# Kernel tuning notes

Measured on AMD Instinct MI355X. Metric: run time of the kernel, lower is better.

## Reference

```python
import jax, jax.numpy as jnp
import numpy as np

B, T, D = 256, 336, 128
H = 1024
N_LABEL, LABEL_CLASS = 24, 1
FORGET_BIAS = 1.0  # TF BasicLSTMCell default


def setup_inputs() -> dict:
    key = jax.random.key(0)
    ks = jax.random.split(key, 8)
    s1 = 1.0 / np.sqrt(D + H)
    s2 = 1.0 / np.sqrt(2 * H)
    sd = 1.0 / np.sqrt(H)
    return {
        "features": jax.random.normal(ks[0], (B, T, D), jnp.float32),
        "labels": jax.random.normal(ks[1], (B, N_LABEL, LABEL_CLASS), jnp.float32),
        "W1": jax.random.normal(ks[2], (D + H, 4 * H), jnp.float32) * s1,
        "b1": jnp.zeros((4 * H,), jnp.float32),
        "W2": jax.random.normal(ks[3], (2 * H, 4 * H), jnp.float32) * s2,
        "b2": jnp.zeros((4 * H,), jnp.float32),
        "Wd": jax.random.normal(ks[4], (H, N_LABEL * LABEL_CLASS), jnp.float32) * sd,
        "bd": jnp.zeros((N_LABEL * LABEL_CLASS,), jnp.float32),
    }


def _lstm_cell(c, h, x, W, b):
    # TF BasicLSTMCell: gates = [x, h] @ W + b, split into i, j, f, o
    z = jnp.concatenate([x, h], axis=-1) @ W + b
    i, j, f, o = jnp.split(z, 4, axis=-1)
    new_c = c * jax.nn.sigmoid(f + FORGET_BIAS) + jax.nn.sigmoid(i) * jnp.tanh(j)
    new_h = jnp.tanh(new_c) * jax.nn.sigmoid(o)
    return new_c, new_h


def reference(features, labels, W1, b1, W2, b2, Wd, bd):
    batch = features.shape[0]
    zeros = jnp.zeros((batch, H), features.dtype)
    init = (zeros, zeros, zeros, zeros)  # c1, h1, c2, h2

    def step(carry, x_t):
        c1, h1, c2, h2 = carry
        c1, h1 = _lstm_cell(c1, h1, x_t, W1, b1)
        c2, h2 = _lstm_cell(c2, h2, h1, W2, b2)
        return (c1, h1, c2, h2), None

    xs = jnp.swapaxes(features, 0, 1)  # [T, B, D]
    (c1, h1, c2, h2), _ = jax.lax.scan(step, init, xs)
    # dense head on last-timestep output of top layer
    pred = (h2 @ Wd + bd).reshape(batch, N_LABEL, LABEL_CLASS)
    loss = jnp.mean(jnp.square(pred - labels))
    return loss
```

## Files before the change

### kernel.cpp

```cpp
#include <hip/hip_runtime.h>

#define TT 336
#define BB 256
#define DD 128
#define HH 1024
#define TD 43008
#define BBHH 262144

#define SSU0 20480u
#define SSU1 32768u
#define LBU1 5242880u

#define ZTS 132

typedef __attribute__((ext_vector_type(8))) short short8;
typedef __attribute__((ext_vector_type(8))) unsigned short ushort8;
typedef __attribute__((ext_vector_type(4))) unsigned short ushort4v;
typedef __attribute__((ext_vector_type(4))) float floatx4;

#define OFF_ZPAD 0u
#define OFF_BAR  4096u
#define OFF_H1   2101248u
#define OFF_H2   3149824u
#define OFF_B1P  4198400u
#define OFF_B2P  4214784u
#define OFF_X    4231168u
#define OFF_BP   26251264u

static __device__ __forceinline__ unsigned short f2bf(float f) {
  unsigned int x = __float_as_uint(f);
  x += 0x7fffu + ((x >> 16) & 1u);
  return (unsigned short)(x >> 16);
}
static __device__ __forceinline__ float bf2f(unsigned short u) {
  return __uint_as_float(((unsigned int)u) << 16);
}
static __device__ __forceinline__ float sigm(float x) {
  return 1.f / (1.f + __expf(-x));
}
static __device__ __forceinline__ float tanh_fast(float x) {
  float ax = fabsf(x);
  float e = __expf(-2.f * ax);
  float t = (1.f - e) / (1.f + e);
  return x < 0.f ? -t : t;
}

#define GLOAD_LDS16(gsrc, ldst)                                              \
  __builtin_amdgcn_global_load_lds(                                          \
      (const __attribute__((address_space(1))) void*)(gsrc),                 \
      (__attribute__((address_space(3))) void*)(ldst), 16, 0, 0)
#define GLOAD_LDS16_DC(gsrc, ldst)                                           \
  __builtin_amdgcn_global_load_lds(                                          \
      (const __attribute__((address_space(1))) void*)(gsrc),                 \
      (__attribute__((address_space(3))) void*)(ldst), 16, 0, 17)

#define ASM_MEMBAR asm volatile("" ::: "memory")

__global__ __launch_bounds__(256) void init_zero(float* out, uint4* span, long n16) {
  long i = (long)blockIdx.x * 256 + threadIdx.x;
  if (i < n16) span[i] = make_uint4(0u, 0u, 0u, 0u);
  if (i == 0) out[0] = 0.f;
}

__global__ __launch_bounds__(256) void feat2bf(const float* __restrict__ in,
                                               unsigned short* __restrict__ out, long nq) {
  long Q = (long)blockIdx.x * 256 + threadIdx.x;
  if (Q >= nq) return;
  int b = (int)(Q / 5376);
  long outQ = (Q & ~7L) | ((Q ^ (long)b) & 7);
  const floatx4* pp = (const floatx4*)(in + Q * 8);
  floatx4 a = pp[0], c = pp[1];
  ushort8 v;
  #pragma unroll
  for (int q = 0; q < 4; ++q) { v[q] = f2bf(a[q]); v[4 + q] = f2bf(c[q]); }
  *(ushort8*)(out + outQ * 8) = v;
}

__global__ __launch_bounds__(256) void bpack(const float* __restrict__ W1,
                                             const float* __restrict__ W2,
                                             unsigned short* __restrict__ out) {
  __shared__ unsigned short tile[64][72];
  int bid = blockIdx.x, t = threadIdx.x;
  int L, tk, tn;
  if (bid < 1280) { L = 0; tk = bid % 20; tn = bid / 20; }
  else            { L = 1; tk = (bid - 1280) % 32; tn = (bid - 1280) / 32; }
  const float* W = L ? W2 : W1;
  int KG = L ? 512 : 320;
  int k0 = tk * 64, n0p = tn * 64;
  int g = k0 / KG;
  int ksg0 = (k0 - g * KG) >> 5;
  int ntile = n0p >> 7, wn = (n0p >> 6) & 1;
  unsigned int SSu = L ? SSU1 : SSU0;
  unsigned int base = (L ? LBU1 : 0u) + ntile * 8u * SSu + (g * 2 + wn) * SSu;

  #pragma unroll
  for (int i = 0; i < 16; ++i) {
    int idx = i * 256 + t;
    int kk = idx >> 6, nn = idx & 63;
    int np = n0p + nn;
    int norig = ((np & 3) << 10) + (np >> 2);
    float v = 0.f;
    if (!(L == 0 && k0 + kk >= 1152)) v = W[(size_t)(k0 + kk) * 4096 + norig];
    tile[kk][nn] = f2bf(v);
  }
  __syncthreads();
  int t64 = t & 63;
  #pragma unroll
  for (int pass = 0; pass < 2; ++pass) {
    int f = (t >> 6) + pass * 4;
    int ksl = f >> 2, ni = f & 3;
    ushort8 v;
    #pragma unroll
    for (int j = 0; j < 8; ++j)
      v[j] = tile[ksl * 32 + ((t64 >> 4) << 3) + j][ni * 16 + (t64 & 15)];
    *(ushort8*)(out + base + (unsigned)((ksg0 + ksl) * 4 + ni) * 512u + t64 * 8) = v;
  }
}

__global__ __launch_bounds__(256) void bias_perm(const float* __restrict__ b1,
                                                 const float* __restrict__ b2,
                                                 float* __restrict__ b1p,
                                                 float* __restrict__ b2p) {
  int idx = blockIdx.x * 256 + threadIdx.x;
  const float* src = (idx < 4096) ? b1 : b2;
  float* dst = (idx < 4096) ? b1p : b2p;
  int n = idx & 4095;
  dst[n] = src[(n & 3) * 1024 + (n >> 2)];
}

__global__ __launch_bounds__(512, 2) void lstm_persist(
    const unsigned short* __restrict__ Xbf,
    unsigned short* __restrict__ h1bufs, unsigned short* __restrict__ h2bufs,
    const unsigned short* __restrict__ Bpack,
    const float* __restrict__ b1p, const float* __restrict__ b2p,
    const unsigned short* __restrict__ zpad,
    unsigned int* __restrict__ bar) {
  __shared__ __align__(16) unsigned short Abuf[4][3][64 * 64];
  __shared__ int sflags[4][2];
  float* zt0 = (float*)&Abuf[0][0][0];
  float* zt1 = zt0 + 64 * ZTS;

  int bid = blockIdx.x;
  int xs = bid & 7;
  int layer = xs >> 2;
  int lid = ((bid >> 3) << 2) | (xs & 3);
  int ntile = (lid & 7) | (((lid >> 5) & 3) << 3);
  int mtile = (lid >> 3) & 3;
  int m0 = mtile * 64;
  int u0 = ntile * 32;
  const int NIT = layer ? 8 : 5;

  int tid = threadIdx.x;
  int g = tid >> 7;
  int wn = (tid >> 6) & 1;
  int lane = tid & 63;
  int kgbase = g * (layer ? 512 : 320);

  unsigned int SSu = layer ? SSU1 : SSU0;
  const unsigned short* bwave =
      Bpack + (layer ? LBU1 : 0u) + ntile * 8u * SSu + (unsigned)(g * 2 + wn) * SSu;

  int r = tid >> 3, ug = tid & 7;
  int rgc = m0 + r;
  const float* bp = (layer ? b2p : b1p) + (size_t)(u0 + ug * 4) * 4;
  floatx4 breg[4];
  #pragma unroll
  for (int k = 0; k < 4; ++k) breg[k] = *(const floatx4*)&bp[k * 4];
  floatx4 creg = (floatx4){0.f, 0.f, 0.f, 0.f};

  unsigned int* gctr = bar;
  unsigned int* xctr = bar + 16 * (1 + (bid & 7));

  if (tid < 8) sflags[tid >> 1][tid & 1] = 0;
  __syncthreads();

  ushort8 bc[2][4], bn[2][4];
  auto loadB = [&](ushort8 (&dst)[2][4], int it) {
    #pragma unroll
    for (int ksl = 0; ksl < 2; ++ksl)
      #pragma unroll
      for (int ni = 0; ni < 4; ++ni)
        dst[ksl][ni] =
            *(const ushort8*)(bwave + (unsigned)((it * 2 + ksl) * 4 + ni) * 512u + lane * 8);
  };

  loadB(bc, 0);
  ASM_MEMBAR;

  for (int p = 0; p <= TT; ++p) {
    bool active = layer ? (p >= 1) : (p < TT);
    if (active) {
      const unsigned short* hp1 = h1bufs + (size_t)(p & 1) * BBHH;
      const unsigned short* hp2 = h2bufs + (size_t)(p & 1) * BBHH;
      int acts = layer ? (p - 1) : p;
      int fbase = acts * NIT;
      volatile int* myf = (volatile int*)&sflags[g][wn];
      volatile int* paf = (volatile int*)&sflags[g][wn ^ 1];

      auto stageA = [&](int buf, int it) {
        int kb = kgbase + (it << 6);
        unsigned short* dst0 = &Abuf[g][buf][0];
        #pragma unroll
        for (int c = 0; c < 4; ++c) {
          int rowbase = c * 16 + wn * 8;
          int rg = m0 + rowbase + (lane >> 3);
          int kq = lane & 7;
          if (layer == 0) {
            if (kb < DD) {
              GLOAD_LDS16(Xbf + (size_t)rg * TD + p * DD + kb + kq * 8,
                          dst0 + rowbase * 64);
            } else if (kb < 1152) {
              GLOAD_LDS16_DC(hp1 + (size_t)rg * HH + (kb - DD) + kq * 8,
                             dst0 + rowbase * 64);
            } else {
              GLOAD_LDS16(zpad + lane * 8, dst0 + rowbase * 64);
            }
          } else {
            if (kb < HH) {
              GLOAD_LDS16_DC(hp1 + (size_t)rg * HH + kb + kq * 8,
                             dst0 + rowbase * 64);
            } else {
              GLOAD_LDS16_DC(hp2 + (size_t)rg * HH + (kb - HH) + kq * 8,
                             dst0 + rowbase * 64);
            }
          }
        }
      };

      floatx4 acc[4][4];
      #pragma unroll
      for (int i = 0; i < 4; ++i)
        #pragma unroll
        for (int j = 0; j < 4; ++j) acc[i][j] = (floatx4){0.f, 0.f, 0.f, 0.f};

      auto computeIt = [&](int buf, ushort8 (&bb)[2][4]) {
        const unsigned short* Ab = &Abuf[g][buf][0];
        #pragma unroll
        for (int ksl = 0; ksl < 2; ++ksl) {
          int qb = ksl * 4 + (lane >> 4);
          short8 af[4];
          #pragma unroll
          for (int mi = 0; mi < 4; ++mi) {
            int ml = mi * 16 + (lane & 15);
            af[mi] = *(const short8*)&Ab[ml * 64 + ((qb ^ (ml & 7)) << 3)];
          }
          #pragma unroll
          for (int mi = 0; mi < 4; ++mi)
            #pragma unroll
            for (int ni = 0; ni < 4; ++ni)
              acc[mi][ni] = __builtin_amdgcn_mfma_f32_16x16x32_bf16(
                  af[mi], (short8)bb[ksl][ni], acc[mi][ni], 0, 0, 0);
        }
      };

      stageA(0, 0);
      ASM_MEMBAR;
      stageA(1, 1);
      ASM_MEMBAR;

      for (int it = 0; it < NIT; ++it) {
        if (it < NIT - 1) {
          asm volatile("s_waitcnt vmcnt(4)" ::: "memory");
        } else {
          asm volatile("s_waitcnt vmcnt(0)" ::: "memory");
        }
        if (lane == 0) *myf = fbase + it + 1;
        ASM_MEMBAR;
        if (it + 1 < NIT) { loadB(bn, it + 1); ASM_MEMBAR; }
        while (*paf < fbase + it + 1) __builtin_amdgcn_s_sleep(1);
        ASM_MEMBAR;
        if (it + 2 < NIT) { stageA((it + 2) % 3, it + 2); ASM_MEMBAR; }
        computeIt(it % 3, bc);
        if (it + 1 < NIT) {
          #pragma unroll
          for (int ksl = 0; ksl < 2; ++ksl)
            #pragma unroll
            for (int ni = 0; ni < 4; ++ni) bc[ksl][ni] = bn[ksl][ni];
        }
      }

      asm volatile("s_waitcnt lgkmcnt(0)" ::: "memory");
      __builtin_amdgcn_s_barrier();
      __builtin_amdgcn_sched_barrier(0);

      float* ztw = (g & 1) ? zt1 : zt0;
      if (g < 2) {
        #pragma unroll
        for (int mi = 0; mi < 4; ++mi)
          #pragma unroll
          for (int ni = 0; ni < 4; ++ni)
            #pragma unroll
            for (int rr = 0; rr < 4; ++rr) {
              int row = mi * 16 + (lane >> 4) * 4 + rr;
              int col = wn * 64 + ni * 16 + (lane & 15);
              ztw[row * ZTS + col] = acc[mi][ni][rr];
            }
      }
      __syncthreads();
      if (g >= 2) {
        #pragma unroll
        for (int mi = 0; mi < 4; ++mi)
          #pragma unroll
          for (int ni = 0; ni < 4; ++ni)
            #pragma unroll
            for (int rr = 0; rr < 4; ++rr) {
              int row = mi * 16 + (lane >> 4) * 4 + rr;
              int col = wn * 64 + ni * 16 + (lane & 15);
              ztw[row * ZTS + col] += acc[mi][ni][rr];
            }
      }
      __syncthreads();

      {
        unsigned short* hn = (layer ? h2bufs : h1bufs) + (size_t)((p + 1) & 1) * BBHH;
        floatx4 cold = creg, cn;
        ushort4v hv;
        #pragma unroll
        for (int k = 0; k < 4; ++k) {
          int cbase = r * ZTS + (ug * 4 + k) * 4;
          floatx4 gt0 = *(const floatx4*)&zt0[cbase];
          floatx4 gt1 = *(const floatx4*)&zt1[cbase];
          floatx4 bb = breg[k];
          float i_ = gt0[0] + gt1[0] + bb[0];
          float j_ = gt0[1] + gt1[1] + bb[1];
          float f_ = gt0[2] + gt1[2] + bb[2] + 1.f;
          float o_ = gt0[3] + gt1[3] + bb[3];
          float nc = cold[k] * sigm(f_) + sigm(i_) * tanh_fast(j_);
          cn[k] = nc;
          hv[k] = f2bf(tanh_fast(nc) * sigm(o_));
        }
        creg = cn;
        int q = (u0 >> 3) + (ug >> 1);
        union { ushort4v v; unsigned long long u; } cu;
        cu.v = hv;
        unsigned long long* hdst = (unsigned long long*)
            &hn[(size_t)rgc * HH + (((q & ~7) | ((q ^ rgc) & 7)) << 3) + (ug & 1) * 4];
        __hip_atomic_store(hdst, cu.u, __ATOMIC_RELAXED, __HIP_MEMORY_SCOPE_AGENT);
      }
      ASM_MEMBAR;

      loadB(bc, 0);
      ASM_MEMBAR;
      asm volatile("s_waitcnt vmcnt(8)" ::: "memory");
    }

    __builtin_amdgcn_s_barrier();
    if (tid == 0) {
      __hip_atomic_fetch_add(xctr, 1u, __ATOMIC_RELAXED, __HIP_MEMORY_SCOPE_AGENT);
      if (bid < 8) {
        unsigned int wantx = 32u * (unsigned int)(p + 1);
        while (__hip_atomic_load(xctr, __ATOMIC_RELAXED, __HIP_MEMORY_SCOPE_AGENT) < wantx)
          __builtin_amdgcn_s_sleep(1);
        __hip_atomic_fetch_add(gctr, 1u, __ATOMIC_RELAXED, __HIP_MEMORY_SCOPE_AGENT);
      }
      unsigned int want = 8u * (unsigned int)(p + 1);
      while (__hip_atomic_load(gctr, __ATOMIC_RELAXED, __HIP_MEMORY_SCOPE_AGENT) < want)
        __builtin_amdgcn_s_sleep(1);
    }
    __builtin_amdgcn_s_barrier();
    ASM_MEMBAR;
  }
  asm volatile("s_waitcnt vmcnt(0)" ::: "memory");
}

__global__ __launch_bounds__(64) void head_loss(const unsigned short* __restrict__ h2,
                                                const float* __restrict__ Wd,
                                                const float* __restrict__ bd,
                                                const float* __restrict__ labels,
                                                float* __restrict__ out) {
  int b = blockIdx.x;
  int l = threadIdx.x;
  float pacc[24];
  #pragma unroll
  for (int n = 0; n < 24; ++n) pacc[n] = 0.f;
  for (int k = l; k < HH; k += 64) {
    int ksw = (k & ~63) | ((((k >> 3) ^ b) & 7) << 3) | (k & 7);
    float hv = bf2f(h2[(size_t)b * HH + ksw]);
    const float* wr = Wd + (size_t)k * 24;
    #pragma unroll
    for (int n = 0; n < 24; ++n) pacc[n] += hv * wr[n];
  }
  #pragma unroll
  for (int n = 0; n < 24; ++n) {
    float v = pacc[n];
    for (int off = 32; off > 0; off >>= 1) v += __shfl_down(v, off);
    pacc[n] = v;
  }
  if (l == 0) {
    float s = 0.f;
    #pragma unroll
    for (int n = 0; n < 24; ++n) {
      float pred = pacc[n] + bd[n];
      float d = pred - labels[b * 24 + n];
      s += d * d;
    }
    atomicAdd(out, s * (1.0f / 6144.0f));
  }
}

extern "C" void kernel_launch(void* const* d_in, const int* in_sizes, int n_in,
                              void* d_out, int out_size, void* d_ws, size_t ws_size,
                              hipStream_t stream) {
  const float* features = (const float*)d_in[0];
  const float* labels   = (const float*)d_in[1];
  const float* W1 = (const float*)d_in[2];
  const float* b1 = (const float*)d_in[3];
  const float* W2 = (const float*)d_in[4];
  const float* b2 = (const float*)d_in[5];
  const float* Wd = (const float*)d_in[6];
  const float* bd = (const float*)d_in[7];

  char* ws = (char*)d_ws;
  unsigned short* zpad = (unsigned short*)(ws + OFF_ZPAD);
  unsigned int*   bar  = (unsigned int*)(ws + OFF_BAR);
  unsigned short* h1   = (unsigned short*)(ws + OFF_H1);
  unsigned short* h2   = (unsigned short*)(ws + OFF_H2);
  float*          b1p  = (float*)(ws + OFF_B1P);
  float*          b2p  = (float*)(ws + OFF_B2P);
  unsigned short* Xbf  = (unsigned short*)(ws + OFF_X);
  unsigned short* BP   = (unsigned short*)(ws + OFF_BP);
  float* out = (float*)d_out;

  init_zero<<<1026, 256, 0, stream>>>(out, (uint4*)ws, 262400L);
  feat2bf<<<5376, 256, 0, stream>>>(features, Xbf, 1376256L);
  bpack<<<3328, 256, 0, stream>>>(W1, W2, BP);
  bias_perm<<<32, 256, 0, stream>>>(b1, b2, b1p, b2p);

  lstm_persist<<<256, 512, 0, stream>>>(Xbf, h1, h2, BP, b1p, b2p, zpad, bar);

  head_loss<<<256, 64, 0, stream>>>(h2 + BBHH, Wd, bd, labels, out);
}
```

Baseline: 5.630 ms.

## Triple-buffer B-operand register prefetch with two-iteration lookahead in recurrent GEMM loop

Replaces the double-buffered B-fragment registers (with a copy from next to current each iteration) with three rotating register buffers, unrolling the K loop by three. B is now prefetched two iterations ahead, and the vmcnt wait is raised so more global loads stay in flight. This aims to hide global/L2 latency of the weight stream and drop the register copies, at the cost of more VGPRs, which may lower occupancy or cause spills.

```diff
diff --git a/kernel.cpp b/kernel.cpp
--- a/kernel.cpp
+++ b/kernel.cpp
@@ -174,7 +174,7 @@
   if (tid < 8) sflags[tid >> 1][tid & 1] = 0;
   __syncthreads();
 
-  ushort8 bc[2][4], bn[2][4];
+  ushort8 bA[2][4], bB[2][4], bC[2][4];
   auto loadB = [&](ushort8 (&dst)[2][4], int it) {
     #pragma unroll
     for (int ksl = 0; ksl < 2; ++ksl)
@@ -184,7 +184,7 @@
             *(const ushort8*)(bwave + (unsigned)((it * 2 + ksl) * 4 + ni) * 512u + lane * 8);
   };
 
-  loadB(bc, 0);
+  loadB(bA, 0);
   ASM_MEMBAR;
 
   for (int p = 0; p <= TT; ++p) {
@@ -255,29 +255,34 @@
 
       stageA(0, 0);
       ASM_MEMBAR;
+      loadB(bB, 1);
+      ASM_MEMBAR;
       stageA(1, 1);
       ASM_MEMBAR;
 
-      for (int it = 0; it < NIT; ++it) {
-        if (it < NIT - 1) {
-          asm volatile("s_waitcnt vmcnt(4)" ::: "memory");
-        } else {
-          asm volatile("s_waitcnt vmcnt(0)" ::: "memory");
-        }
-        if (lane == 0) *myf = fbase + it + 1;
-        ASM_MEMBAR;
-        if (it + 1 < NIT) { loadB(bn, it + 1); ASM_MEMBAR; }
-        while (*paf < fbase + it + 1) __builtin_amdgcn_s_sleep(1);
-        ASM_MEMBAR;
-        if (it + 2 < NIT) { stageA((it + 2) % 3, it + 2); ASM_MEMBAR; }
-        computeIt(it % 3, bc);
-        if (it + 1 < NIT) {
-          #pragma unroll
-          for (int ksl = 0; ksl < 2; ++ksl)
-            #pragma unroll
-            for (int ni = 0; ni < 4; ++ni) bc[ksl][ni] = bn[ksl][ni];
-        }
-      }
+#define KBODY(bX, bZ, jj, CS, SS)                                            \
+      {                                                                      \
+        int j_ = (jj);                                                       \
+        if (j_ < NIT - 1) {                                                  \
+          asm volatile("s_waitcnt vmcnt(12)" ::: "memory");                  \
+        } else {                                                             \
+          asm volatile("s_waitcnt vmcnt(0)" ::: "memory");                   \
+        }                                                                    \
+        if (lane == 0) *myf = fbase + j_ + 1;                                \
+        ASM_MEMBAR;                                                          \
+        if (j_ + 2 < NIT) { loadB(bZ, j_ + 2); ASM_MEMBAR; }                 \
+        while (*paf < fbase + j_ + 1) __builtin_amdgcn_s_sleep(1);           \
+        ASM_MEMBAR;                                                          \
+        if (j_ + 2 < NIT) { stageA((SS), j_ + 2); ASM_MEMBAR; }              \
+        computeIt((CS), bX);                                                 \
+      }
+
+      for (int j = 0; j < NIT; j += 3) {
+        KBODY(bA, bC, j, 0, 2);
+        if (j + 1 < NIT) KBODY(bB, bA, j + 1, 1, 0);
+        if (j + 2 < NIT) KBODY(bC, bB, j + 2, 2, 1);
+      }
+#undef KBODY
 
       asm volatile("s_waitcnt lgkmcnt(0)" ::: "memory");
       __builtin_amdgcn_s_barrier();
@@ -339,7 +344,7 @@
       }
       ASM_MEMBAR;
 
-      loadB(bc, 0);
+      loadB(bA, 0);
       ASM_MEMBAR;
       asm volatile("s_waitcnt vmcnt(8)" ::: "memory");
     }
```

New measurement: 5.961 ms. 1.06x slower.
